# Performance work log

Measured on AMD Instinct MI355X. Metric: run time of the kernel, lower is better.

## Reference

```python
import jax, jax.numpy as jnp
import numpy as np

B, S, D = 8, 2048, 2048  # seq_len must equal dim for this module's math to type-check


def setup_inputs() -> dict:
    key = jax.random.key(0)
    ks = jax.random.split(key, 9)
    sc = 1.0 / np.sqrt(D)
    return {
        "query": jax.random.normal(ks[0], (B, S, D), jnp.float32),
        "key_": jax.random.normal(ks[1], (B, S, D), jnp.float32),
        "value": jax.random.normal(ks[2], (B, S, D), jnp.float32),
        "Wq": jax.random.normal(ks[3], (D, D), jnp.float32) * sc,
        "bq": jax.random.normal(ks[4], (D,), jnp.float32) * 0.01,
        "Wk": jax.random.normal(ks[5], (D, D), jnp.float32) * sc,
        "bk": jax.random.normal(ks[6], (D,), jnp.float32) * 0.01,
        "Wv": jax.random.normal(ks[7], (D, D), jnp.float32) * sc,
        "bv": jax.random.normal(ks[8], (D,), jnp.float32) * 0.01,
    }


def reference(query, key_, value, Wq, bq, Wk, bk, Wv, bv):
    scale_factor = 1.0  # forward default
    # Linear projections (torch Linear: x @ W^T + b)
    q = jnp.einsum('bsd,ed->bse', query, Wq) + bq   # [B,S,D]
    k = jnp.einsum('bsd,ed->bse', key_, Wk) + bk    # [B,S,D]
    v = jnp.einsum('bsd,ed->bse', value, Wv) + bv   # [B,S,D]
    # Transpose last two dims, then matmul: [B,D,S] @ [B,D,S] (valid since S == D)
    qT = jnp.swapaxes(q, -2, -1)
    kT = jnp.swapaxes(k, -2, -1)
    qk = jnp.matmul(qT, kT) * scale_factor          # [B,D,S]
    attn = jax.nn.softmax(qk, axis=-1)
    # dropout_p = 0 -> identity
    out = jnp.matmul(attn, v)                       # [B,D,D]
    return jnp.swapaxes(out, -2, -1)
```

## Files before the change

kernel.cpp:

```cpp
#include <hip/hip_runtime.h>
#include <hip/hip_fp16.h>


using half8_t = __attribute__((ext_vector_type(8))) _Float16;
using f32x4   = __attribute__((ext_vector_type(4))) float;

static constexpr int NB = 8;
static constexpr int Sd = 2048;
static constexpr long MAT = (long)Sd * Sd;

__device__ __forceinline__ void gload16(const _Float16* g, _Float16* l) {
  __builtin_amdgcn_global_load_lds(
      (const __attribute__((address_space(1))) void*)g,
      (__attribute__((address_space(3))) void*)l, 16, 0, 0);
}
#define VMCNT(n) asm volatile("s_waitcnt vmcnt(" #n ")")
#define BAR()    __builtin_amdgcn_s_barrier()
#define SCHEDB() __builtin_amdgcn_sched_barrier(0)

template<bool SPLIT>
__global__ __launch_bounds__(256) void presplit(const float* __restrict__ in,
    _Float16* __restrict__ h, _Float16* __restrict__ l, long n8, float scl)
{
  long i = (long)blockIdx.x * 256 + threadIdx.x;
  const long stride = (long)gridDim.x * 256;
  for (; i < n8; i += stride) {
    const f32x4* p = (const f32x4*)(in + i * 8);
    f32x4 a = p[0], b = p[1];
    half8_t hh, ll;
#pragma unroll
    for (int j = 0; j < 4; j++) {
      float x = a[j] * scl; _Float16 hv = (_Float16)x;
      hh[j] = hv; if constexpr (SPLIT) ll[j] = (_Float16)(x - (float)hv);
      float y = b[j] * scl; _Float16 hw = (_Float16)y;
      hh[4 + j] = hw; if constexpr (SPLIT) ll[4 + j] = (_Float16)(y - (float)hw);
    }
    *(half8_t*)(h + i * 8) = hh;
    if constexpr (SPLIT) *(half8_t*)(l + i * 8) = ll;
  }
}

template<int NSEG, int BIAS, int OUT>
__global__ __launch_bounds__(512, 2) void gemm8(
    const _Float16* __restrict__ Ah, const _Float16* __restrict__ Al, long sA,
    const _Float16* __restrict__ Bh, long sB,
    const float* __restrict__ bias, float cscale,
    void* __restrict__ Cp, void* __restrict__ Clp, long sC)
{
  constexpr int H = NSEG * 64;
  __shared__ __align__(16) _Float16 LA[4][8192];
  __shared__ __align__(16) _Float16 LB[4][8192];

  const int t = threadIdx.x, w = t >> 6, l = t & 63;

  const int wg = blockIdx.x;
  const int swz = (wg & 7) * 64 + (wg >> 3);
  const int bz = swz >> 6, rem = swz & 63;
  const int by = rem >> 3, bx = rem & 7;

  const _Float16* PAh = Ah + (size_t)bz * sA + (size_t)(by * 256) * Sd;
  const _Float16* PBh = Bh + (size_t)bz * sB + (size_t)(bx * 256) * Sd;
  const _Float16* PAl = (NSEG == 2)
      ? Al + (size_t)bz * sA + (size_t)(by * 256) * Sd : PAh;

  const int s7 = t & 7;
  const int lkS = (s7 >> 1) ^ ((t >> 3) & 3);
  const size_t srcoff = (size_t)(2 * (t >> 3) + (s7 & 1)) * Sd + lkS * 8;
  const int du0 = w * 512;

  const int wm = (w >> 2) * 128, wn = (w & 3) * 64;
  const int lm = l & 15, lkr = l >> 4;
  const int sprime = ((lkr ^ ((lm >> 1) & 3)) << 1) | (lm & 1);
  const int aoff = (wm >> 1) * 128 + (lm >> 1) * 128 + sprime * 16;
  const int boff = (wn >> 1) * 128 + (lm >> 1) * 128 + sprime * 16;

  auto srcA = [&](int hp) -> const _Float16* {
    if constexpr (NSEG == 2) return (hp >> 6) ? PAl : PAh;
    return PAh;
  };
  auto koOf = [&](int hp) -> int {
    if constexpr (NSEG == 2) return (hp & 63) * 32;
    return hp * 32;
  };
  auto stageU = [&](int hp) {
    const int uu = hp & 3;
    const _Float16* a = srcA(hp) + koOf(hp);
    const _Float16* b = PBh + koOf(hp);
    gload16(a + srcoff, LA[uu] + du0);
    gload16(a + srcoff + (size_t)128 * Sd, LA[uu] + du0 + 4096);
    gload16(b + srcoff, LB[uu] + du0);
    gload16(b + srcoff + (size_t)128 * Sd, LB[uu] + du0 + 4096);
  };

  f32x4 acc[8][4] = {};
  half8_t a0[8], b0[4], a1[8], b1[4];

  auto readF = [&](int slot, half8_t (&fa)[8], half8_t (&fb)[4]) {
#pragma unroll
    for (int f = 0; f < 8; f++)
      fa[f] = *(const half8_t*)((const char*)LA[slot] + aoff + f * 1024);
#pragma unroll
    for (int n = 0; n < 4; n++)
      fb[n] = *(const half8_t*)((const char*)LB[slot] + boff + n * 1024);
  };
  auto mfma32 = [&](const half8_t (&fa)[8], const half8_t (&fb)[4]) {
    __builtin_amdgcn_s_setprio(1);
#pragma unroll
    for (int f = 0; f < 8; f++)
#pragma unroll
      for (int n = 0; n < 4; n++)
        acc[f][n] = __builtin_amdgcn_mfma_f32_16x16x32_f16(fa[f], fb[n], acc[f][n], 0, 0, 0);
    __builtin_amdgcn_s_setprio(0);
  };

  stageU(0); stageU(1); stageU(2);
  VMCNT(4);
  BAR();
  readF(0, a0, b0);

  for (int j = 0; j < H / 2; ++j) {
    {
      const int u = 2 * j;
      readF((u + 1) & 3, a1, b1);
      SCHEDB();
      mfma32(a0, b0);
      SCHEDB();
      if (u + 3 < H) { stageU(u + 3); VMCNT(4); }
      BAR();
    }
    {
      const int u = 2 * j + 1;
      if (u + 1 < H) readF((u + 1) & 3, a0, b0);
      SCHEDB();
      mfma32(a1, b1);
      SCHEDB();
      if (u + 3 < H)      { stageU(u + 3); VMCNT(4); }
      else if (u == H - 3) { VMCNT(0); }
      if (u + 1 < H) BAR();
    }
  }

  const int row_base = by * 256 + wm + (lkr << 2);
  const int col_base = bx * 256 + wn + lm;
#pragma unroll
  for (int fm = 0; fm < 8; fm++)
#pragma unroll
    for (int fn = 0; fn < 4; fn++) {
      const int n = col_base + fn * 16;
      float bcol = 0.f;
      if constexpr (BIAS == 1) bcol = bias[n];
#pragma unroll
      for (int r = 0; r < 4; r++) {
        const int m = row_base + fm * 16 + r;
        float v = acc[fm][fn][r] * cscale;
        if constexpr (BIAS == 1) v += bcol;
        if constexpr (BIAS == 2) v += bias[m];
        const size_t ci = (size_t)bz * sC + (size_t)m * Sd + n;
        if constexpr (OUT == 0) ((float*)Cp)[ci] = v;
        else if constexpr (OUT == 1) ((_Float16*)Cp)[ci] = (_Float16)v;
        else if constexpr (OUT == 3) ((_Float16*)Cp)[ci] = (_Float16)(v * 16.0f);
        else {
          float sv = v * 16.0f;
          _Float16 hv = (_Float16)sv;
          ((_Float16*)Cp)[ci]  = hv;
          ((_Float16*)Clp)[ci] = (_Float16)(sv - (float)hv);
        }
      }
    }
}

__global__ __launch_bounds__(256) void softmax_rows(const float* __restrict__ X,
                                                    _Float16* __restrict__ P)
{
  __shared__ float red[4];
  const size_t row = blockIdx.x;
  const float* x = X + row * Sd;
  _Float16* p = P + row * Sd;
  const int t = threadIdx.x;
  float v[8];
  float mx = -1e30f;
#pragma unroll
  for (int i = 0; i < 8; i++) { v[i] = x[t + 256 * i]; mx = fmaxf(mx, v[i]); }
#pragma unroll
  for (int o = 32; o > 0; o >>= 1) mx = fmaxf(mx, __shfl_xor(mx, o, 64));
  if ((t & 63) == 0) red[t >> 6] = mx;
  __syncthreads();
  mx = fmaxf(fmaxf(red[0], red[1]), fmaxf(red[2], red[3]));
  __syncthreads();
  float s = 0.f;
#pragma unroll
  for (int i = 0; i < 8; i++) { v[i] = __expf(v[i] - mx); s += v[i]; }
#pragma unroll
  for (int o = 32; o > 0; o >>= 1) s += __shfl_xor(s, o, 64);
  if ((t & 63) == 0) red[t >> 6] = s;
  __syncthreads();
  s = red[0] + red[1] + red[2] + red[3];
  float inv = 1.f / s;
#pragma unroll
  for (int i = 0; i < 8; i++) p[t + 256 * i] = (_Float16)(v[i] * inv);
}

extern "C" void kernel_launch(void* const* d_in, const int* in_sizes, int n_in,
                              void* d_out, int out_size, void* d_ws, size_t ws_size,
                              hipStream_t stream)
{
  const float* query = (const float*)d_in[0];
  const float* key_  = (const float*)d_in[1];
  const float* value = (const float*)d_in[2];
  const float* Wq = (const float*)d_in[3];
  const float* bq = (const float*)d_in[4];
  const float* Wk = (const float*)d_in[5];
  const float* bk = (const float*)d_in[6];
  const float* Wv = (const float*)d_in[7];
  const float* bv = (const float*)d_in[8];

  char* ws = (char*)d_ws;
  char* ob = (char*)d_out;
  const size_t M64 = (size_t)NB * MAT * 2;

  _Float16* q_h  = (_Float16*)(ws);
  _Float16* k_h  = (_Float16*)(ws);
  _Float16* k_l  = (_Float16*)(ws + M64);
  float*    qk   = (float*)(ws);
  _Float16* qT_h = (_Float16*)(ws + 2 * M64);
  _Float16* qT_l = (_Float16*)(ws + 3 * M64);
  _Float16* P    = qT_h;
  _Float16* vT   = qT_l;
  _Float16* kk_h = (_Float16*)(ws + 4 * M64);
  _Float16* val_h = (_Float16*)(ws + 5 * M64);

  _Float16* wq_h = (_Float16*)(ob);
  _Float16* wq_l = (_Float16*)(ob + (MAT * 2));
  _Float16* wk_h = (_Float16*)(ob + 2 * (MAT * 2));
  _Float16* wv_h = (_Float16*)(ob + 3 * (MAT * 2));
  float* out = (float*)d_out;

  dim3 blk256(256), blk512(512);
  dim3 gg(512);
  const long NQ8 = (long)NB * MAT / 8;
  const long NW8 = MAT / 8;

  presplit<false><<<dim3(2048), blk256, 0, stream>>>(query, q_h, nullptr, NQ8, 16.f);
  presplit<true><<<dim3(2048), blk256, 0, stream>>>(Wq, wq_h, wq_l, NW8, 16.f);
  gemm8<2, 2, 2><<<gg, blk512, 0, stream>>>(wq_h, wq_l, 0, q_h, MAT,
                                            bq, 1.f / 256.f, qT_h, qT_l, MAT);
  presplit<true><<<dim3(2048), blk256, 0, stream>>>(key_, k_h, k_l, NQ8, 16.f);
  presplit<false><<<dim3(2048), blk256, 0, stream>>>(Wk, wk_h, nullptr, NW8, 16.f);
  gemm8<2, 1, 3><<<gg, blk512, 0, stream>>>(k_h, k_l, MAT, wk_h, 0,
                                            bk, 1.f / 256.f, kk_h, nullptr, MAT);
  gemm8<2, 0, 0><<<gg, blk512, 0, stream>>>(qT_h, qT_l, MAT, kk_h, MAT,
                                            nullptr, 1.f / 256.f, qk, nullptr, MAT);
  softmax_rows<<<dim3(NB * Sd), blk256, 0, stream>>>(qk, P);
  presplit<false><<<dim3(2048), blk256, 0, stream>>>(value, val_h, nullptr, NQ8, 1.f);
  presplit<false><<<dim3(2048), blk256, 0, stream>>>(Wv, wv_h, nullptr, NW8, 1.f);
  gemm8<1, 2, 1><<<gg, blk512, 0, stream>>>(wv_h, nullptr, 0, val_h, MAT,
                                            bv, 1.f, vT, nullptr, MAT);
  gemm8<1, 0, 0><<<gg, blk512, 0, stream>>>(vT, nullptr, MAT, P, MAT,
                                            nullptr, 1.f, out, nullptr, MAT);
}
```

Measured before the change: 1.265 ms.

## Shrink GEMM tiles to 128x128 with 4 waves and 32x32x16 MFMAs

Replaces the 256x256-tile, 8-wave GEMM with a 128x128-tile, 4-wave kernel that uses 32x32x16 f16 MFMA instructions, a new LDS layout without the XOR swizzle, and a grid of 2048 blocks. The goal is more blocks per CU and better load balance, plus the higher-throughput larger MFMA shape. In exchange, each tile reuses its data less, so global/L2 traffic rises, and the unswizzled LDS reads may hit bank conflicts.

```diff
diff --git a/kernel.cpp b/kernel.cpp
--- a/kernel.cpp
+++ b/kernel.cpp
@@ -4,6 +4,7 @@
 
 using half8_t = __attribute__((ext_vector_type(8))) _Float16;
 using f32x4   = __attribute__((ext_vector_type(4))) float;
+using f32x16  = __attribute__((ext_vector_type(16))) float;
 
 static constexpr int NB = 8;
 static constexpr int Sd = 2048;
@@ -41,38 +42,36 @@
 }
 
 template<int NSEG, int BIAS, int OUT>
-__global__ __launch_bounds__(512, 2) void gemm8(
+__global__ __launch_bounds__(256, 2) void gemm9(
     const _Float16* __restrict__ Ah, const _Float16* __restrict__ Al, long sA,
     const _Float16* __restrict__ Bh, long sB,
     const float* __restrict__ bias, float cscale,
     void* __restrict__ Cp, void* __restrict__ Clp, long sC)
 {
   constexpr int H = NSEG * 64;
-  __shared__ __align__(16) _Float16 LA[4][8192];
-  __shared__ __align__(16) _Float16 LB[4][8192];
+  __shared__ __align__(16) _Float16 LA[4][4096];
+  __shared__ __align__(16) _Float16 LB[4][4096];
 
   const int t = threadIdx.x, w = t >> 6, l = t & 63;
 
   const int wg = blockIdx.x;
-  const int swz = (wg & 7) * 64 + (wg >> 3);
-  const int bz = swz >> 6, rem = swz & 63;
-  const int by = rem >> 3, bx = rem & 7;
-
-  const _Float16* PAh = Ah + (size_t)bz * sA + (size_t)(by * 256) * Sd;
-  const _Float16* PBh = Bh + (size_t)bz * sB + (size_t)(bx * 256) * Sd;
+  const int swz = (wg & 7) * 256 + (wg >> 3);
+  const int bz = swz >> 8, rem = swz & 255;
+  const int by = rem >> 4, bx = rem & 15;
+
+  const _Float16* PAh = Ah + (size_t)bz * sA + (size_t)(by * 128) * Sd;
+  const _Float16* PBh = Bh + (size_t)bz * sB + (size_t)(bx * 128) * Sd;
   const _Float16* PAl = (NSEG == 2)
-      ? Al + (size_t)bz * sA + (size_t)(by * 256) * Sd : PAh;
-
-  const int s7 = t & 7;
-  const int lkS = (s7 >> 1) ^ ((t >> 3) & 3);
-  const size_t srcoff = (size_t)(2 * (t >> 3) + (s7 & 1)) * Sd + lkS * 8;
+      ? Al + (size_t)bz * sA + (size_t)(by * 128) * Sd : PAh;
+
+  const size_t srcoff = (size_t)(((t >> 6) << 4) | (t & 15)) * Sd
+                      + (size_t)(((t >> 4) & 3) * 8);
   const int du0 = w * 512;
 
-  const int wm = (w >> 2) * 128, wn = (w & 3) * 64;
-  const int lm = l & 15, lkr = l >> 4;
-  const int sprime = ((lkr ^ ((lm >> 1) & 3)) << 1) | (lm & 1);
-  const int aoff = (wm >> 1) * 128 + (lm >> 1) * 128 + sprime * 16;
-  const int boff = (wn >> 1) * 128 + (lm >> 1) * 128 + sprime * 16;
+  const int wm = (w >> 1) * 64, wn = (w & 1) * 64;
+  const int laneoff = ((l >> 4) & 1) * 1024 + (l >> 5) * 256 + (l & 15) * 16;
+  const int aoff = wm * 64 + laneoff;
+  const int boff = wn * 64 + laneoff;
 
   auto srcA = [&](int hp) -> const _Float16* {
     if constexpr (NSEG == 2) return (hp >> 6) ? PAl : PAh;
@@ -87,29 +86,33 @@
     const _Float16* a = srcA(hp) + koOf(hp);
     const _Float16* b = PBh + koOf(hp);
     gload16(a + srcoff, LA[uu] + du0);
-    gload16(a + srcoff + (size_t)128 * Sd, LA[uu] + du0 + 4096);
+    gload16(a + srcoff + (size_t)64 * Sd, LA[uu] + du0 + 2048);
     gload16(b + srcoff, LB[uu] + du0);
-    gload16(b + srcoff + (size_t)128 * Sd, LB[uu] + du0 + 4096);
-  };
-
-  f32x4 acc[8][4] = {};
-  half8_t a0[8], b0[4], a1[8], b1[4];
-
-  auto readF = [&](int slot, half8_t (&fa)[8], half8_t (&fb)[4]) {
-#pragma unroll
-    for (int f = 0; f < 8; f++)
-      fa[f] = *(const half8_t*)((const char*)LA[slot] + aoff + f * 1024);
-#pragma unroll
-    for (int n = 0; n < 4; n++)
-      fb[n] = *(const half8_t*)((const char*)LB[slot] + boff + n * 1024);
-  };
-  auto mfma32 = [&](const half8_t (&fa)[8], const half8_t (&fb)[4]) {
+    gload16(b + srcoff + (size_t)64 * Sd, LB[uu] + du0 + 2048);
+  };
+
+  f32x16 acc[2][2] = {};
+  half8_t a0[4], b0[4], a1[4], b1[4];
+
+  auto readF = [&](int slot, half8_t (&fa)[4], half8_t (&fb)[4]) {
+#pragma unroll
+    for (int fm = 0; fm < 2; fm++)
+#pragma unroll
+      for (int ks = 0; ks < 2; ks++) {
+        fa[fm * 2 + ks] = *(const half8_t*)((const char*)LA[slot] + aoff + fm * 2048 + ks * 512);
+        fb[fm * 2 + ks] = *(const half8_t*)((const char*)LB[slot] + boff + fm * 2048 + ks * 512);
+      }
+  };
+  auto mfma8 = [&](const half8_t (&fa)[4], const half8_t (&fb)[4]) {
     __builtin_amdgcn_s_setprio(1);
 #pragma unroll
-    for (int f = 0; f < 8; f++)
-#pragma unroll
-      for (int n = 0; n < 4; n++)
-        acc[f][n] = __builtin_amdgcn_mfma_f32_16x16x32_f16(fa[f], fb[n], acc[f][n], 0, 0, 0);
+    for (int ks = 0; ks < 2; ks++)
+#pragma unroll
+      for (int fm = 0; fm < 2; fm++)
+#pragma unroll
+        for (int fn = 0; fn < 2; fn++)
+          acc[fm][fn] = __builtin_amdgcn_mfma_f32_32x32x16_f16(
+              fa[fm * 2 + ks], fb[fn * 2 + ks], acc[fm][fn], 0, 0, 0);
     __builtin_amdgcn_s_setprio(0);
   };
 
@@ -123,35 +126,34 @@
       const int u = 2 * j;
       readF((u + 1) & 3, a1, b1);
       SCHEDB();
-      mfma32(a0, b0);
-      SCHEDB();
-      if (u + 3 < H) { stageU(u + 3); VMCNT(4); }
-      BAR();
+      mfma8(a0, b0);
+      SCHEDB();
+      if (u + 3 < H) { stageU(u + 3); VMCNT(4); BAR(); }
     }
     {
       const int u = 2 * j + 1;
       if (u + 1 < H) readF((u + 1) & 3, a0, b0);
       SCHEDB();
-      mfma32(a1, b1);
-      SCHEDB();
-      if (u + 3 < H)      { stageU(u + 3); VMCNT(4); }
-      else if (u == H - 3) { VMCNT(0); }
-      if (u + 1 < H) BAR();
+      mfma8(a1, b1);
+      SCHEDB();
+      if (u + 3 < H)       { stageU(u + 3); VMCNT(4); BAR(); }
+      else if (u == H - 3) { VMCNT(0); BAR(); }
     }
   }
 
-  const int row_base = by * 256 + wm + (lkr << 2);
-  const int col_base = bx * 256 + wn + lm;
-#pragma unroll
-  for (int fm = 0; fm < 8; fm++)
-#pragma unroll
-    for (int fn = 0; fn < 4; fn++) {
-      const int n = col_base + fn * 16;
+  const int hi = l >> 5;
+  const int colb = bx * 128 + wn + (l & 31);
+  const int rowb = by * 128 + wm + 4 * hi;
+#pragma unroll
+  for (int fm = 0; fm < 2; fm++)
+#pragma unroll
+    for (int fn = 0; fn < 2; fn++) {
+      const int n = colb + fn * 32;
       float bcol = 0.f;
       if constexpr (BIAS == 1) bcol = bias[n];
 #pragma unroll
-      for (int r = 0; r < 4; r++) {
-        const int m = row_base + fm * 16 + r;
+      for (int r = 0; r < 16; r++) {
+        const int m = rowb + fm * 32 + (r & 3) + 8 * (r >> 2);
         float v = acc[fm][fn][r] * cscale;
         if constexpr (BIAS == 1) v += bcol;
         if constexpr (BIAS == 2) v += bias[m];
@@ -235,26 +237,26 @@
   _Float16* wv_h = (_Float16*)(ob + 3 * (MAT * 2));
   float* out = (float*)d_out;
 
-  dim3 blk256(256), blk512(512);
-  dim3 gg(512);
+  dim3 blk256(256);
+  dim3 gg(2048);
   const long NQ8 = (long)NB * MAT / 8;
   const long NW8 = MAT / 8;
 
   presplit<false><<<dim3(2048), blk256, 0, stream>>>(query, q_h, nullptr, NQ8, 16.f);
   presplit<true><<<dim3(2048), blk256, 0, stream>>>(Wq, wq_h, wq_l, NW8, 16.f);
-  gemm8<2, 2, 2><<<gg, blk512, 0, stream>>>(wq_h, wq_l, 0, q_h, MAT,
+  gemm9<2, 2, 2><<<gg, blk256, 0, stream>>>(wq_h, wq_l, 0, q_h, MAT,
                                             bq, 1.f / 256.f, qT_h, qT_l, MAT);
   presplit<true><<<dim3(2048), blk256, 0, stream>>>(key_, k_h, k_l, NQ8, 16.f);
   presplit<false><<<dim3(2048), blk256, 0, stream>>>(Wk, wk_h, nullptr, NW8, 16.f);
-  gemm8<2, 1, 3><<<gg, blk512, 0, stream>>>(k_h, k_l, MAT, wk_h, 0,
+  gemm9<2, 1, 3><<<gg, blk256, 0, stream>>>(k_h, k_l, MAT, wk_h, 0,
                                             bk, 1.f / 256.f, kk_h, nullptr, MAT);
-  gemm8<2, 0, 0><<<gg, blk512, 0, stream>>>(qT_h, qT_l, MAT, kk_h, MAT,
+  gemm9<2, 0, 0><<<gg, blk256, 0, stream>>>(qT_h, qT_l, MAT, kk_h, MAT,
                                             nullptr, 1.f / 256.f, qk, nullptr, MAT);
   softmax_rows<<<dim3(NB * Sd), blk256, 0, stream>>>(qk, P);
   presplit<false><<<dim3(2048), blk256, 0, stream>>>(value, val_h, nullptr, NQ8, 1.f);
   presplit<false><<<dim3(2048), blk256, 0, stream>>>(Wv, wv_h, nullptr, NW8, 1.f);
-  gemm8<1, 2, 1><<<gg, blk512, 0, stream>>>(wv_h, nullptr, 0, val_h, MAT,
+  gemm9<1, 2, 1><<<gg, blk256, 0, stream>>>(wv_h, nullptr, 0, val_h, MAT,
                                             bv, 1.f, vT, nullptr, MAT);
-  gemm8<1, 0, 0><<<gg, blk512, 0, stream>>>(vT, nullptr, MAT, P, MAT,
+  gemm9<1, 0, 0><<<gg, blk256, 0, stream>>>(vT, nullptr, MAT, P, MAT,
                                             nullptr, 1.f, out, nullptr, MAT);
 }
```

Result: slower. 2.105 ms (+66.4%).

## Stagger two wave groups one k-step apart with five-slot LDS ring in GEMM

Applied to the files above, without the earlier changes.

Restructures the GEMM main loop so the two groups of four waves run offset by one k-step: group 0 computes the current tile while prefetching fragments, and group 1 reads and computes the previous slot. The wave-to-tile mapping is changed so each group owns half of the N columns, and the LDS ring grows from four to five slots so both groups' slots stay live. The aim is to spread LDS reads and MFMA bursts across the waves so they overlap better and contend less. In exchange it uses more LDS per block (which may hurt two-blocks-per-CU occupancy), adds an extra loop iteration, and group 1 waits on lgkmcnt(0) before its MFMAs.

```diff
diff --git a/kernel.cpp b/kernel.cpp
--- a/kernel.cpp
+++ b/kernel.cpp
@@ -14,9 +14,11 @@
       (const __attribute__((address_space(1))) void*)g,
       (__attribute__((address_space(3))) void*)l, 16, 0, 0);
 }
-#define VMCNT(n) asm volatile("s_waitcnt vmcnt(" #n ")")
-#define BAR()    __builtin_amdgcn_s_barrier()
+__device__ __forceinline__ void barrier_() { asm volatile("s_barrier" ::: "memory"); }
+__device__ __forceinline__ void lgkm0_()   { asm volatile("s_waitcnt lgkmcnt(0)" ::: "memory"); }
+#define VMCNT(n) asm volatile("s_waitcnt vmcnt(" #n ")" ::: "memory")
 #define SCHEDB() __builtin_amdgcn_sched_barrier(0)
+#define INC5(x) x = ((x) == 4 ? 0 : (x) + 1)
 
 template<bool SPLIT>
 __global__ __launch_bounds__(256) void presplit(const float* __restrict__ in,
@@ -41,17 +43,18 @@
 }
 
 template<int NSEG, int BIAS, int OUT>
-__global__ __launch_bounds__(512, 2) void gemm8(
+__global__ __launch_bounds__(512, 2) void gemm12(
     const _Float16* __restrict__ Ah, const _Float16* __restrict__ Al, long sA,
     const _Float16* __restrict__ Bh, long sB,
     const float* __restrict__ bias, float cscale,
     void* __restrict__ Cp, void* __restrict__ Clp, long sC)
 {
   constexpr int H = NSEG * 64;
-  __shared__ __align__(16) _Float16 LA[4][8192];
-  __shared__ __align__(16) _Float16 LB[4][8192];
+  __shared__ __align__(16) _Float16 LA[5][8192];
+  __shared__ __align__(16) _Float16 LB[5][8192];
 
   const int t = threadIdx.x, w = t >> 6, l = t & 63;
+  const int grp = w >> 2;
 
   const int wg = blockIdx.x;
   const int swz = (wg & 7) * 64 + (wg >> 3);
@@ -68,7 +71,8 @@
   const size_t srcoff = (size_t)(2 * (t >> 3) + (s7 & 1)) * Sd + lkS * 8;
   const int du0 = w * 512;
 
-  const int wm = (w >> 2) * 128, wn = (w & 3) * 64;
+  const int wq2 = w & 3;
+  const int wm = (wq2 >> 1) * 128, wn = (wq2 & 1) * 64 + grp * 128;
   const int lm = l & 15, lkr = l >> 4;
   const int sprime = ((lkr ^ ((lm >> 1) & 3)) << 1) | (lm & 1);
   const int aoff = (wm >> 1) * 128 + (lm >> 1) * 128 + sprime * 16;
@@ -82,18 +86,17 @@
     if constexpr (NSEG == 2) return (hp & 63) * 32;
     return hp * 32;
   };
-  auto stageU = [&](int hp) {
-    const int uu = hp & 3;
+  auto stageP = [&](int hp, int slot) {
     const _Float16* a = srcA(hp) + koOf(hp);
     const _Float16* b = PBh + koOf(hp);
-    gload16(a + srcoff, LA[uu] + du0);
-    gload16(a + srcoff + (size_t)128 * Sd, LA[uu] + du0 + 4096);
-    gload16(b + srcoff, LB[uu] + du0);
-    gload16(b + srcoff + (size_t)128 * Sd, LB[uu] + du0 + 4096);
+    gload16(a + srcoff, LA[slot] + du0);
+    gload16(a + srcoff + (size_t)128 * Sd, LA[slot] + du0 + 4096);
+    gload16(b + srcoff, LB[slot] + du0);
+    gload16(b + srcoff + (size_t)128 * Sd, LB[slot] + du0 + 4096);
   };
 
   f32x4 acc[8][4] = {};
-  half8_t a0[8], b0[4], a1[8], b1[4];
+  half8_t fa0[8], fb0[4], fa1[8], fb1[4];
 
   auto readF = [&](int slot, half8_t (&fa)[8], half8_t (&fb)[4]) {
 #pragma unroll
@@ -113,32 +116,35 @@
     __builtin_amdgcn_s_setprio(0);
   };
 
-  stageU(0); stageU(1); stageU(2);
+  stageP(0, 0); stageP(1, 1); stageP(2, 2);
   VMCNT(4);
-  BAR();
-  readF(0, a0, b0);
-
-  for (int j = 0; j < H / 2; ++j) {
-    {
-      const int u = 2 * j;
-      readF((u + 1) & 3, a1, b1);
-      SCHEDB();
-      mfma32(a0, b0);
-      SCHEDB();
-      if (u + 3 < H) { stageU(u + 3); VMCNT(4); }
-      BAR();
-    }
-    {
-      const int u = 2 * j + 1;
-      if (u + 1 < H) readF((u + 1) & 3, a0, b0);
-      SCHEDB();
-      mfma32(a1, b1);
-      SCHEDB();
-      if (u + 3 < H)      { stageU(u + 3); VMCNT(4); }
-      else if (u == H - 3) { VMCNT(0); }
-      if (u + 1 < H) BAR();
-    }
+  barrier_();
+  if (grp == 0) readF(0, fa0, fb0);
+
+  int sm1 = 4, sp1 = 1, sp3 = 3;
+
+#define ITER(J, CONS_A, CONS_B, NEXT_A, NEXT_B)                               \
+  {                                                                           \
+    const int j_ = (J);                                                       \
+    if (grp == 0) {                                                           \
+      if (j_ < H) { SCHEDB(); mfma32(CONS_A, CONS_B); SCHEDB(); }             \
+      if (j_ + 1 < H) readF(sp1, NEXT_A, NEXT_B);                             \
+    } else {                                                                  \
+      if (j_ >= 1) {                                                          \
+        readF(sm1, fa0, fb0); lgkm0_(); SCHEDB(); mfma32(fa0, fb0); SCHEDB(); \
+      }                                                                       \
+    }                                                                         \
+    if (j_ + 3 < H)       { stageP(j_ + 3, sp3); VMCNT(4); }                  \
+    else if (j_ + 3 == H) { VMCNT(0); }                                       \
+    if (j_ < H) barrier_();                                                   \
+    INC5(sm1); INC5(sp1); INC5(sp3);                                          \
   }
+
+  for (int j = 0; j <= H; j += 2) {
+    ITER(j, fa0, fb0, fa1, fb1)
+    if (j + 1 <= H) ITER(j + 1, fa1, fb1, fa0, fb0)
+  }
+#undef ITER
 
   const int row_base = by * 256 + wm + (lkr << 2);
   const int col_base = bx * 256 + wn + lm;
@@ -242,19 +248,19 @@
 
   presplit<false><<<dim3(2048), blk256, 0, stream>>>(query, q_h, nullptr, NQ8, 16.f);
   presplit<true><<<dim3(2048), blk256, 0, stream>>>(Wq, wq_h, wq_l, NW8, 16.f);
-  gemm8<2, 2, 2><<<gg, blk512, 0, stream>>>(wq_h, wq_l, 0, q_h, MAT,
-                                            bq, 1.f / 256.f, qT_h, qT_l, MAT);
+  gemm12<2, 2, 2><<<gg, blk512, 0, stream>>>(wq_h, wq_l, 0, q_h, MAT,
+                                             bq, 1.f / 256.f, qT_h, qT_l, MAT);
   presplit<true><<<dim3(2048), blk256, 0, stream>>>(key_, k_h, k_l, NQ8, 16.f);
   presplit<false><<<dim3(2048), blk256, 0, stream>>>(Wk, wk_h, nullptr, NW8, 16.f);
-  gemm8<2, 1, 3><<<gg, blk512, 0, stream>>>(k_h, k_l, MAT, wk_h, 0,
-                                            bk, 1.f / 256.f, kk_h, nullptr, MAT);
-  gemm8<2, 0, 0><<<gg, blk512, 0, stream>>>(qT_h, qT_l, MAT, kk_h, MAT,
-                                            nullptr, 1.f / 256.f, qk, nullptr, MAT);
+  gemm12<2, 1, 3><<<gg, blk512, 0, stream>>>(k_h, k_l, MAT, wk_h, 0,
+                                             bk, 1.f / 256.f, kk_h, nullptr, MAT);
+  gemm12<2, 0, 0><<<gg, blk512, 0, stream>>>(qT_h, qT_l, MAT, kk_h, MAT,
+                                             nullptr, 1.f / 256.f, qk, nullptr, MAT);
   softmax_rows<<<dim3(NB * Sd), blk256, 0, stream>>>(qk, P);
   presplit<false><<<dim3(2048), blk256, 0, stream>>>(value, val_h, nullptr, NQ8, 1.f);
   presplit<false><<<dim3(2048), blk256, 0, stream>>>(Wv, wv_h, nullptr, NW8, 1.f);
-  gemm8<1, 2, 1><<<gg, blk512, 0, stream>>>(wv_h, nullptr, 0, val_h, MAT,
-                                            bv, 1.f, vT, nullptr, MAT);
-  gemm8<1, 0, 0><<<gg, blk512, 0, stream>>>(vT, nullptr, MAT, P, MAT,
-                                            nullptr, 1.f, out, nullptr, MAT);
-}
+  gemm12<1, 2, 1><<<gg, blk512, 0, stream>>>(wv_h, nullptr, 0, val_h, MAT,
+                                             bv, 1.f, vT, nullptr, MAT);
+  gemm12<1, 0, 0><<<gg, blk512, 0, stream>>>(vT, nullptr, MAT, P, MAT,
+                                             nullptr, 1.f, out, nullptr, MAT);
+}
```

Result: slower. 1.548 ms (+22.4%).

## Switch GEMM to 32x32x16 MFMA tiles and reuse B fragments across split-A segments

Applied to the files above, without the earlier changes.

Rewrites the GEMM inner kernel to use 32x32x16 MFMA instructions with a 2x4 per-wave tile over a new LDS layout and lane mapping. For the split-precision case it interleaves the hi and lo A panels per K step, so each B tile is loaded once and used for both segments instead of being reloaded in a second pass. The aim is fewer B global loads and LDS reads per FLOP, plus a more efficient MFMA shape. The cost is a new, unswizzled LDS layout that may cause bank conflicts, and more complex wait-count bookkeeping that could go wrong.

```diff
diff --git a/kernel.cpp b/kernel.cpp
--- a/kernel.cpp
+++ b/kernel.cpp
@@ -4,6 +4,7 @@
 
 using half8_t = __attribute__((ext_vector_type(8))) _Float16;
 using f32x4   = __attribute__((ext_vector_type(4))) float;
+using f32x16  = __attribute__((ext_vector_type(16))) float;
 
 static constexpr int NB = 8;
 static constexpr int Sd = 2048;
@@ -14,8 +15,8 @@
       (const __attribute__((address_space(1))) void*)g,
       (__attribute__((address_space(3))) void*)l, 16, 0, 0);
 }
-#define VMCNT(n) asm volatile("s_waitcnt vmcnt(" #n ")")
-#define BAR()    __builtin_amdgcn_s_barrier()
+__device__ __forceinline__ void barrier_() { asm volatile("s_barrier" ::: "memory"); }
+#define VMCNT(n) asm volatile("s_waitcnt vmcnt(" #n ")" ::: "memory")
 #define SCHEDB() __builtin_amdgcn_sched_barrier(0)
 
 template<bool SPLIT>
@@ -41,13 +42,13 @@
 }
 
 template<int NSEG, int BIAS, int OUT>
-__global__ __launch_bounds__(512, 2) void gemm8(
+__global__ __launch_bounds__(512, 2) void gemm13(
     const _Float16* __restrict__ Ah, const _Float16* __restrict__ Al, long sA,
     const _Float16* __restrict__ Bh, long sB,
     const float* __restrict__ bias, float cscale,
     void* __restrict__ Cp, void* __restrict__ Clp, long sC)
 {
-  constexpr int H = NSEG * 64;
+  constexpr int H = 64;
   __shared__ __align__(16) _Float16 LA[4][8192];
   __shared__ __align__(16) _Float16 LB[4][8192];
 
@@ -63,96 +64,134 @@
   const _Float16* PAl = (NSEG == 2)
       ? Al + (size_t)bz * sA + (size_t)(by * 256) * Sd : PAh;
 
-  const int s7 = t & 7;
-  const int lkS = (s7 >> 1) ^ ((t >> 3) & 3);
-  const size_t srcoff = (size_t)(2 * (t >> 3) + (s7 & 1)) * Sd + lkS * 8;
+  const size_t srcoff = (size_t)(w * 16 + (l & 15)) * Sd + (size_t)((l >> 4) * 8);
   const int du0 = w * 512;
 
-  const int wm = (w >> 2) * 128, wn = (w & 3) * 64;
-  const int lm = l & 15, lkr = l >> 4;
-  const int sprime = ((lkr ^ ((lm >> 1) & 3)) << 1) | (lm & 1);
-  const int aoff = (wm >> 1) * 128 + (lm >> 1) * 128 + sprime * 16;
-  const int boff = (wn >> 1) * 128 + (lm >> 1) * 128 + sprime * 16;
-
-  auto srcA = [&](int hp) -> const _Float16* {
-    if constexpr (NSEG == 2) return (hp >> 6) ? PAl : PAh;
-    return PAh;
-  };
-  auto koOf = [&](int hp) -> int {
-    if constexpr (NSEG == 2) return (hp & 63) * 32;
-    return hp * 32;
-  };
-  auto stageU = [&](int hp) {
-    const int uu = hp & 3;
-    const _Float16* a = srcA(hp) + koOf(hp);
-    const _Float16* b = PBh + koOf(hp);
-    gload16(a + srcoff, LA[uu] + du0);
-    gload16(a + srcoff + (size_t)128 * Sd, LA[uu] + du0 + 4096);
-    gload16(b + srcoff, LB[uu] + du0);
-    gload16(b + srcoff + (size_t)128 * Sd, LB[uu] + du0 + 4096);
-  };
-
-  f32x4 acc[8][4] = {};
-  half8_t a0[8], b0[4], a1[8], b1[4];
-
-  auto readF = [&](int slot, half8_t (&fa)[8], half8_t (&fb)[4]) {
-#pragma unroll
-    for (int f = 0; f < 8; f++)
-      fa[f] = *(const half8_t*)((const char*)LA[slot] + aoff + f * 1024);
-#pragma unroll
-    for (int n = 0; n < 4; n++)
-      fb[n] = *(const half8_t*)((const char*)LB[slot] + boff + n * 1024);
-  };
-  auto mfma32 = [&](const half8_t (&fa)[8], const half8_t (&fb)[4]) {
+  const int wm = (w >> 1) * 64, wn = (w & 1) * 128;
+  const int laneoff = ((l >> 4) & 1) * 1024 + (l >> 5) * 256 + (l & 15) * 16;
+  const int aoff = wm * 64 + laneoff;
+  const int boff = wn * 64 + laneoff;
+
+  auto stageA = [&](int p) {
+    const int slot = p & 3;
+    const _Float16* base;
+    if constexpr (NSEG == 2)
+      base = ((p & 1) ? PAl : PAh) + (p >> 1) * 32;
+    else
+      base = PAh + p * 32;
+    gload16(base + srcoff, LA[slot] + du0);
+    gload16(base + srcoff + (size_t)128 * Sd, LA[slot] + du0 + 4096);
+  };
+  auto stageB = [&](int k) {
+    const int slot = k & 3;
+    const _Float16* base = PBh + k * 32;
+    gload16(base + srcoff, LB[slot] + du0);
+    gload16(base + srcoff + (size_t)128 * Sd, LB[slot] + du0 + 4096);
+  };
+
+  f32x16 acc[2][4] = {};
+  half8_t a0[4], a1[4], b[8];
+
+  auto readA = [&](int slot, half8_t (&fa)[4]) {
+#pragma unroll
+    for (int rt = 0; rt < 2; rt++)
+#pragma unroll
+      for (int ks = 0; ks < 2; ks++)
+        fa[rt * 2 + ks] =
+            *(const half8_t*)((const char*)LA[slot] + aoff + rt * 2048 + ks * 512);
+  };
+  auto readB = [&](int slot) {
+#pragma unroll
+    for (int ct = 0; ct < 4; ct++)
+#pragma unroll
+      for (int ks = 0; ks < 2; ks++)
+        b[ct * 2 + ks] =
+            *(const half8_t*)((const char*)LB[slot] + boff + ct * 2048 + ks * 512);
+  };
+  auto mfma16 = [&](const half8_t (&fa)[4]) {
     __builtin_amdgcn_s_setprio(1);
 #pragma unroll
-    for (int f = 0; f < 8; f++)
-#pragma unroll
-      for (int n = 0; n < 4; n++)
-        acc[f][n] = __builtin_amdgcn_mfma_f32_16x16x32_f16(fa[f], fb[n], acc[f][n], 0, 0, 0);
+    for (int ks = 0; ks < 2; ks++)
+#pragma unroll
+      for (int rt = 0; rt < 2; rt++)
+#pragma unroll
+        for (int ct = 0; ct < 4; ct++)
+          acc[rt][ct] = __builtin_amdgcn_mfma_f32_32x32x16_f16(
+              fa[rt * 2 + ks], b[ct * 2 + ks], acc[rt][ct], 0, 0, 0);
     __builtin_amdgcn_s_setprio(0);
   };
 
-  stageU(0); stageU(1); stageU(2);
-  VMCNT(4);
-  BAR();
-  readF(0, a0, b0);
-
-  for (int j = 0; j < H / 2; ++j) {
-    {
-      const int u = 2 * j;
-      readF((u + 1) & 3, a1, b1);
+  if constexpr (NSEG == 2) {
+    stageA(0); stageB(0); stageA(1); stageA(2); stageB(1);
+    VMCNT(4);
+    barrier_();
+    readA(0, a0);
+
+    for (int k = 0; k < H; ++k) {
+      readA((2 * k + 1) & 3, a1);
+      readB(k & 3);
+      if (k + 2 < H)      { stageA(2 * k + 3); stageB(k + 2); }
+      else if (k + 1 < H) { stageA(2 * k + 3); }
       SCHEDB();
-      mfma32(a0, b0);
+      mfma16(a0);
+      if (k + 2 < H)      { VMCNT(4); }
+      else if (k + 1 < H) { VMCNT(2); }
+      else                { VMCNT(0); }
+      barrier_();
+      if (k + 1 < H) readA((2 * k + 2) & 3, a0);
+      if (k + 2 < H) stageA(2 * k + 4);
       SCHEDB();
-      if (u + 3 < H) { stageU(u + 3); VMCNT(4); }
-      BAR();
-    }
-    {
-      const int u = 2 * j + 1;
-      if (u + 1 < H) readF((u + 1) & 3, a0, b0);
-      SCHEDB();
-      mfma32(a1, b1);
-      SCHEDB();
-      if (u + 3 < H)      { stageU(u + 3); VMCNT(4); }
-      else if (u == H - 3) { VMCNT(0); }
-      if (u + 1 < H) BAR();
+      mfma16(a1);
+      if (k + 2 < H)      { VMCNT(2); }
+      else if (k + 1 < H) { VMCNT(0); }
+      if (k + 1 < H) barrier_();
+    }
+  } else {
+    stageA(0); stageB(0); stageA(1); stageB(1); stageA(2); stageB(2);
+    VMCNT(6);
+    barrier_();
+    readA(0, a0);
+
+    for (int j = 0; j < H / 2; ++j) {
+      {
+        const int u = 2 * j;
+        readA((u + 1) & 3, a1);
+        readB(u & 3);
+        if (u + 3 < H) { stageA(u + 3); stageB(u + 3); }
+        SCHEDB();
+        mfma16(a0);
+        if (u + 3 < H)       { VMCNT(4); }
+        else if (u + 3 == H) { VMCNT(0); }
+        barrier_();
+      }
+      {
+        const int u = 2 * j + 1;
+        if (u + 1 < H) readA((u + 1) & 3, a0);
+        readB(u & 3);
+        if (u + 3 < H) { stageA(u + 3); stageB(u + 3); }
+        SCHEDB();
+        mfma16(a1);
+        if (u + 3 < H)       { VMCNT(4); }
+        else if (u + 3 == H) { VMCNT(0); }
+        if (u + 1 < H) barrier_();
+      }
     }
   }
 
-  const int row_base = by * 256 + wm + (lkr << 2);
-  const int col_base = bx * 256 + wn + lm;
-#pragma unroll
-  for (int fm = 0; fm < 8; fm++)
-#pragma unroll
-    for (int fn = 0; fn < 4; fn++) {
-      const int n = col_base + fn * 16;
+  const int hi = l >> 5;
+  const int colb = bx * 256 + wn + (l & 31);
+  const int rowb = by * 256 + wm + 4 * hi;
+#pragma unroll
+  for (int rt = 0; rt < 2; rt++)
+#pragma unroll
+    for (int ct = 0; ct < 4; ct++) {
+      const int n = colb + ct * 32;
       float bcol = 0.f;
       if constexpr (BIAS == 1) bcol = bias[n];
 #pragma unroll
-      for (int r = 0; r < 4; r++) {
-        const int m = row_base + fm * 16 + r;
-        float v = acc[fm][fn][r] * cscale;
+      for (int r = 0; r < 16; r++) {
+        const int m = rowb + rt * 32 + (r & 3) + 8 * (r >> 2);
+        float v = acc[rt][ct][r] * cscale;
         if constexpr (BIAS == 1) v += bcol;
         if constexpr (BIAS == 2) v += bias[m];
         const size_t ci = (size_t)bz * sC + (size_t)m * Sd + n;
@@ -242,19 +281,19 @@
 
   presplit<false><<<dim3(2048), blk256, 0, stream>>>(query, q_h, nullptr, NQ8, 16.f);
   presplit<true><<<dim3(2048), blk256, 0, stream>>>(Wq, wq_h, wq_l, NW8, 16.f);
-  gemm8<2, 2, 2><<<gg, blk512, 0, stream>>>(wq_h, wq_l, 0, q_h, MAT,
-                                            bq, 1.f / 256.f, qT_h, qT_l, MAT);
+  gemm13<2, 2, 2><<<gg, blk512, 0, stream>>>(wq_h, wq_l, 0, q_h, MAT,
+                                             bq, 1.f / 256.f, qT_h, qT_l, MAT);
   presplit<true><<<dim3(2048), blk256, 0, stream>>>(key_, k_h, k_l, NQ8, 16.f);
   presplit<false><<<dim3(2048), blk256, 0, stream>>>(Wk, wk_h, nullptr, NW8, 16.f);
-  gemm8<2, 1, 3><<<gg, blk512, 0, stream>>>(k_h, k_l, MAT, wk_h, 0,
-                                            bk, 1.f / 256.f, kk_h, nullptr, MAT);
-  gemm8<2, 0, 0><<<gg, blk512, 0, stream>>>(qT_h, qT_l, MAT, kk_h, MAT,
-                                            nullptr, 1.f / 256.f, qk, nullptr, MAT);
+  gemm13<2, 1, 3><<<gg, blk512, 0, stream>>>(k_h, k_l, MAT, wk_h, 0,
+                                             bk, 1.f / 256.f, kk_h, nullptr, MAT);
+  gemm13<2, 0, 0><<<gg, blk512, 0, stream>>>(qT_h, qT_l, MAT, kk_h, MAT,
+                                             nullptr, 1.f / 256.f, qk, nullptr, MAT);
   softmax_rows<<<dim3(NB * Sd), blk256, 0, stream>>>(qk, P);
   presplit<false><<<dim3(2048), blk256, 0, stream>>>(value, val_h, nullptr, NQ8, 1.f);
   presplit<false><<<dim3(2048), blk256, 0, stream>>>(Wv, wv_h, nullptr, NW8, 1.f);
-  gemm8<1, 2, 1><<<gg, blk512, 0, stream>>>(wv_h, nullptr, 0, val_h, MAT,
-                                            bv, 1.f, vT, nullptr, MAT);
-  gemm8<1, 0, 0><<<gg, blk512, 0, stream>>>(vT, nullptr, MAT, P, MAT,
-                                            nullptr, 1.f, out, nullptr, MAT);
-}
+  gemm13<1, 2, 1><<<gg, blk512, 0, stream>>>(wv_h, nullptr, 0, val_h, MAT,
+                                             bv, 1.f, vT, nullptr, MAT);
+  gemm13<1, 0, 0><<<gg, blk512, 0, stream>>>(vT, nullptr, MAT, P, MAT,
+                                             nullptr, 1.f, out, nullptr, MAT);
+}
```

New measurement: 1.306 ms. 1.03x slower.
